# Performance work log

Measured on AMD Instinct MI355X. Metric: run time of the kernel, lower is better.

Reference implementation:

```python
import jax, jax.numpy as jnp
import numpy as np

DIM = 1024
HEADS = 16

def setup_inputs() -> dict:
    key = jax.random.key(0)
    ks = jax.random.split(key, 9)
    s = DIM ** -0.5  # init scale for weights
    x = jax.random.normal(ks[0], (2, 2048, DIM), dtype=jnp.float32)
    wq = jax.random.normal(ks[1], (DIM, DIM), dtype=jnp.float32) * s
    bq = jax.random.normal(ks[2], (DIM,), dtype=jnp.float32) * 0.01
    wk = jax.random.normal(ks[3], (DIM, DIM), dtype=jnp.float32) * s
    bk = jax.random.normal(ks[4], (DIM,), dtype=jnp.float32) * 0.01
    wv = jax.random.normal(ks[5], (DIM, DIM), dtype=jnp.float32) * s
    bv = jax.random.normal(ks[6], (DIM,), dtype=jnp.float32) * 0.01
    wo = jax.random.normal(ks[7], (DIM, DIM), dtype=jnp.float32) * s
    bo = jax.random.normal(ks[8], (DIM,), dtype=jnp.float32) * 0.01
    return {"x": x, "wq": wq, "bq": bq, "wk": wk, "bk": bk,
            "wv": wv, "bv": bv, "wo": wo, "bo": bo}

def reference(x, wq, bq, wk, bk, wv, bv, wo, bo):
    b, l, dim = x.shape
    h = HEADS
    d = dim // h
    scale = dim ** -0.5  # NOTE: full dim, as in the original module
    # torch Linear: x @ W.T + b
    def proj(w, bias):
        y = jnp.einsum('bld,ed->ble', x, w) + bias
        return y.reshape(b, l, h, d).transpose(0, 2, 1, 3)  # b h l d
    q = proj(wq, bq)
    k = proj(wk, bk)
    v = proj(wv, bv)
    attn = jnp.einsum('bhid,bhjd->bhij', q, k) * scale
    attn = jax.nn.softmax(attn, axis=-1)
    out = jnp.einsum('bhij,bhjd->bhid', attn, v)
    out = out.transpose(0, 2, 1, 3).reshape(b, l, dim)
    return jnp.einsum('ble,fe->blf', out, wo) + bo
```

## Files before the change

### kernel.cpp

```cpp
#include <hip/hip_runtime.h>
#include <hip/hip_bf16.h>
#include <stdint.h>


typedef __attribute__((ext_vector_type(8))) short short8;
typedef __attribute__((ext_vector_type(4))) float f32x4;
typedef __attribute__((ext_vector_type(16))) float f32x16;

#define MFMA(a, b, c) __builtin_amdgcn_mfma_f32_16x16x32_bf16((a), (b), (c), 0, 0, 0)
#define MFMA32(a, b, c) __builtin_amdgcn_mfma_f32_32x32x16_bf16((a), (b), (c), 0, 0, 0)

#if __has_builtin(__builtin_amdgcn_exp2f)
#define EXP2(x) __builtin_amdgcn_exp2f(x)
#else
#define EXP2(x) exp2f(x)
#endif

__device__ __forceinline__ ushort f2bf(float f) {
  uint32_t u = __builtin_bit_cast(uint32_t, f);
  u += 0x7fffu + ((u >> 16) & 1u);
  return (ushort)(u >> 16);
}

__device__ __forceinline__ uint32_t pkbf(float lo, float hi) {
  __hip_bfloat162 h = __float22bfloat162_rn(make_float2(lo, hi));
  uint32_t u;
  __builtin_memcpy(&u, &h, 4);
  return u;
}

__device__ __forceinline__ uint32_t cvtpk(float lo, float hi) {
  uint32_t u;
  asm("v_cvt_pk_bf16_f32 %0, %1, %2" : "=v"(u) : "v"(lo), "v"(hi));
  return u;
}

__device__ __forceinline__ void pl32swap(uint32_t& a, uint32_t& b) {
  asm("v_permlane32_swap_b32 %0, %1" : "+v"(a), "+v"(b));
}

__device__ __forceinline__ void gl_lds16(const void* g, void* l) {
  __builtin_amdgcn_global_load_lds(
      (const __attribute__((address_space(1))) unsigned int*)g,
      (__attribute__((address_space(3))) unsigned int*)l, 16, 0, 0);
}

__global__ __launch_bounds__(256) void convert_all(
    const float* __restrict__ x, const float* __restrict__ wq,
    const float* __restrict__ wk, const float* __restrict__ wv,
    const float* __restrict__ wo, ushort* __restrict__ dst) {
  size_t i4 = (size_t)blockIdx.x * 256 + threadIdx.x;
  size_t e = i4 * 4;
  const float* src; size_t off;
  if (e < 4194304u)      { src = x;  off = e; }
  else if (e < 5242880u) { src = wq; off = e - 4194304u; }
  else if (e < 6291456u) { src = wk; off = e - 5242880u; }
  else if (e < 7340032u) { src = wv; off = e - 6291456u; }
  else                   { src = wo; off = e - 7340032u; }
  float4 v = *(const float4*)(src + off);
  ushort4 o = { f2bf(v.x), f2bf(v.y), f2bf(v.z), f2bf(v.w) };
  *(ushort4*)(dst + e) = o;
}

__global__ __launch_bounds__(256) void gemm_qkv(
    const ushort* __restrict__ xb,
    const ushort* __restrict__ wqb, const ushort* __restrict__ wkb,
    const ushort* __restrict__ wvb,
    const float* __restrict__ bq_, const float* __restrict__ bk_,
    const float* __restrict__ bv_,
    ushort* __restrict__ qout, ushort* __restrict__ kout,
    ushort* __restrict__ vtout) {
  __shared__ __align__(16) ushort As[128 * 32];
  __shared__ __align__(16) ushort Bs[128 * 32];
  const int z = blockIdx.z;
  const int bn = blockIdx.x, bm = blockIdx.y;
  const int t = threadIdx.x;
  const int w = t >> 6, lane = t & 63;
  const int wr = w >> 1, wc = w & 1;
  const int l15 = lane & 15, l4 = lane >> 4;

  const ushort* wb = (z == 0) ? wqb : (z == 1 ? wkb : wvb);
  const float* bias = (z == 0) ? bq_ : (z == 1 ? bk_ : bv_);

  f32x4 acc[4][4] = {};

  for (int kt = 0; kt < 32; ++kt) {
    __syncthreads();
#pragma unroll
    for (int rr = 0; rr < 2; ++rr) {
      int c = t + rr * 256;
      int row = c >> 2, cin = c & 3;
      gl_lds16(xb + (bm * 128 + row) * 1024 + kt * 32 + cin * 8, (void*)&As[c * 8]);
      gl_lds16(wb + (bn * 128 + row) * 1024 + kt * 32 + cin * 8, (void*)&Bs[c * 8]);
    }
    __syncthreads();
    short8 af[4], bfr[4];
#pragma unroll
    for (int mf = 0; mf < 4; ++mf)
      af[mf] = *(const short8*)&As[(wr * 64 + mf * 16 + l15) * 32 + l4 * 8];
#pragma unroll
    for (int nf = 0; nf < 4; ++nf)
      bfr[nf] = *(const short8*)&Bs[(wc * 64 + nf * 16 + l15) * 32 + l4 * 8];
    __builtin_amdgcn_s_setprio(1);
#pragma unroll
    for (int mf = 0; mf < 4; ++mf)
#pragma unroll
      for (int nf = 0; nf < 4; ++nf)
        acc[mf][nf] = MFMA(af[mf], bfr[nf], acc[mf][nf]);
    __builtin_amdgcn_s_setprio(0);
  }

  const float qsc = 0.045084439f;
#pragma unroll
  for (int mf = 0; mf < 4; ++mf) {
#pragma unroll
    for (int nf = 0; nf < 4; ++nf) {
      int n = bn * 128 + wc * 64 + nf * 16 + l15;
      int m0 = bm * 128 + wr * 64 + mf * 16 + l4 * 4;
      float b = bias[n];
      float vals[4];
#pragma unroll
      for (int r = 0; r < 4; ++r) vals[r] = acc[mf][nf][r] + b;
      int bb = m0 >> 11, l0 = m0 & 2047;
      int h = n >> 6, d = n & 63;
      int bh = bb * 16 + h;
      if (z == 2) {
        *(uint2*)&vtout[(bh * 64 + d) * 2048 + l0] =
            make_uint2(pkbf(vals[0], vals[1]), pkbf(vals[2], vals[3]));
      } else if (z == 0) {
#pragma unroll
        for (int r = 0; r < 4; ++r)
          qout[(bh * 2048 + l0 + r) * 64 + d] = f2bf(vals[r] * qsc);
      } else {
#pragma unroll
        for (int r = 0; r < 4; ++r)
          kout[(bh * 2048 + l0 + r) * 64 + d] = f2bf(vals[r]);
      }
    }
  }
}

__global__ __launch_bounds__(256, 2) void attn(
    const ushort* __restrict__ qb, const ushort* __restrict__ kb,
    const ushort* __restrict__ vtb, ushort* __restrict__ aout) {
  __shared__ __align__(16) ushort Ks[2][64 * 64];
  __shared__ __align__(16) ushort Vs[2][64 * 64];
  const int bid = blockIdx.x;
  const int xcd = bid & 7, idx = bid >> 3;
  const int bh = xcd * 4 + (idx >> 4);
  const int it = idx & 15;
  const int t = threadIdx.x, w = t >> 6, lane = t & 63;
  const int l31 = lane & 31, hi = lane >> 5;
  const size_t kvbase = (size_t)bh * (2048 * 64);
  const int i0 = it * 128 + w * 32;

  const int c0 = t, c1 = t + 256;
  const int r0 = c0 >> 3, s0 = (c0 & 7) ^ (r0 & 7);
  const int r1 = c1 >> 3, s1 = (c1 & 7) ^ (r1 & 7);

#define STAGE(bufi, jts)                                                     \
  {                                                                          \
    const int j0s = (jts) * 64;                                              \
    gl_lds16(kb + kvbase + (size_t)(j0s + r0) * 64 + s0 * 8,                 \
             (void*)&Ks[bufi][c0 * 8]);                                      \
    gl_lds16(kb + kvbase + (size_t)(j0s + r1) * 64 + s1 * 8,                 \
             (void*)&Ks[bufi][c1 * 8]);                                      \
    gl_lds16(vtb + kvbase + (size_t)r0 * 2048 + j0s + s0 * 8,                \
             (void*)&Vs[bufi][c0 * 8]);                                      \
    gl_lds16(vtb + kvbase + (size_t)r1 * 2048 + j0s + s1 * 8,                \
             (void*)&Vs[bufi][c1 * 8]);                                      \
  }

  short8 qf[4];
#pragma unroll
  for (int ks = 0; ks < 4; ++ks)
    qf[ks] = *(const short8*)&qb[kvbase + (size_t)(i0 + l31) * 64 + ks * 16 + hi * 8];

  f32x16 ot0 = {}, ot1 = {};
  float ts0 = 0.f, ts1 = 0.f, ts2 = 0.f, ts3 = 0.f;

  STAGE(0, 0);
  __syncthreads();

  for (int jt = 0; jt < 32; ++jt) {
    const int cur = jt & 1;
    if (jt < 31) STAGE(cur ^ 1, jt + 1);

    const ushort* Kc = &Ks[cur][0];
    const ushort* Vc = &Vs[cur][0];

    const int swz = (l31 & 7);
    short8 ka0[4], ka1[4], va0[4], va1[4];
#pragma unroll
    for (int ks = 0; ks < 4; ++ks) {
      int ck = (ks * 2 + hi) ^ swz;
      ka0[ks] = *(const short8*)&Kc[l31 * 64 + ck * 8];
      ka1[ks] = *(const short8*)&Kc[(32 + l31) * 64 + ck * 8];
    }
#pragma unroll
    for (int b = 0; b < 4; ++b) {
      int cv = (b * 2 + hi) ^ swz;
      va0[b] = *(const short8*)&Vc[l31 * 64 + cv * 8];
      va1[b] = *(const short8*)&Vc[(32 + l31) * 64 + cv * 8];
    }

    f32x16 st0 = {}, st1 = {};
    __builtin_amdgcn_s_setprio(1);
#pragma unroll
    for (int ks = 0; ks < 4; ++ks) {
      st0 = MFMA32(ka0[ks], qf[ks], st0);
      st1 = MFMA32(ka1[ks], qf[ks], st1);
    }
    __builtin_amdgcn_s_setprio(0);

    f32x16 p0, p1;
#pragma unroll
    for (int r = 0; r < 16; r += 4) {
      p0[r] = EXP2(st0[r]);         ts0 += p0[r];
      p0[r + 1] = EXP2(st0[r + 1]); ts1 += p0[r + 1];
      p0[r + 2] = EXP2(st0[r + 2]); ts2 += p0[r + 2];
      p0[r + 3] = EXP2(st0[r + 3]); ts3 += p0[r + 3];
    }
#pragma unroll
    for (int r = 0; r < 16; r += 4) {
      p1[r] = EXP2(st1[r]);         ts0 += p1[r];
      p1[r + 1] = EXP2(st1[r + 1]); ts1 += p1[r + 1];
      p1[r + 2] = EXP2(st1[r + 2]); ts2 += p1[r + 2];
      p1[r + 3] = EXP2(st1[r + 3]); ts3 += p1[r + 3];
    }

    short8 pb[4];
#pragma unroll
    for (int b = 0; b < 4; ++b) {
      f32x16 pv = (b < 2) ? p0 : p1;
      const int R = 8 * (b & 1);
      uint32_t c01 = cvtpk(pv[R + 0], pv[R + 1]);
      uint32_t c23 = cvtpk(pv[R + 2], pv[R + 3]);
      uint32_t c45 = cvtpk(pv[R + 4], pv[R + 5]);
      uint32_t c67 = cvtpk(pv[R + 6], pv[R + 7]);
      pl32swap(c01, c45);
      pl32swap(c23, c67);
      union { uint32_t u[4]; short8 s; } pk;
      pk.u[0] = c01; pk.u[1] = c23; pk.u[2] = c45; pk.u[3] = c67;
      pb[b] = pk.s;
    }

    __builtin_amdgcn_s_setprio(1);
#pragma unroll
    for (int b = 0; b < 4; ++b) {
      ot0 = MFMA32(va0[b], pb[b], ot0);
      ot1 = MFMA32(va1[b], pb[b], ot1);
    }
    __builtin_amdgcn_s_setprio(0);

    __syncthreads();
  }

  float lsum = (ts0 + ts1) + (ts2 + ts3);
  {
    uint32_t a = __builtin_bit_cast(uint32_t, lsum);
    uint32_t b = a;
    pl32swap(a, b);
    lsum = __builtin_bit_cast(float, a) + __builtin_bit_cast(float, b);
  }
  const int bb = bh >> 4, h = bh & 15;
  float inv = 1.0f / lsum;
  ushort* orow = aout + (size_t)(bb * 2048 + i0 + l31) * 1024 + h * 64;
#pragma unroll
  for (int mf = 0; mf < 2; ++mf) {
    f32x16 o = mf ? ot1 : ot0;
#pragma unroll
    for (int g = 0; g < 4; ++g) {
      int d0 = mf * 32 + g * 8 + hi * 4;
      *(uint2*)(orow + d0) = make_uint2(
          cvtpk(o[g * 4 + 0] * inv, o[g * 4 + 1] * inv),
          cvtpk(o[g * 4 + 2] * inv, o[g * 4 + 3] * inv));
    }
  }
#undef STAGE
}

__global__ __launch_bounds__(256) void gemm_out(
    const ushort* __restrict__ ab, const ushort* __restrict__ wob,
    const float* __restrict__ bo_, float* __restrict__ out) {
  __shared__ __align__(16) ushort As[128 * 32];
  __shared__ __align__(16) ushort Bs[128 * 32];
  const int bn = blockIdx.x, bm = blockIdx.y;
  const int t = threadIdx.x;
  const int w = t >> 6, lane = t & 63;
  const int wr = w >> 1, wc = w & 1;
  const int l15 = lane & 15, l4 = lane >> 4;

  f32x4 acc[4][4] = {};

  for (int kt = 0; kt < 32; ++kt) {
    __syncthreads();
#pragma unroll
    for (int rr = 0; rr < 2; ++rr) {
      int c = t + rr * 256;
      int row = c >> 2, cin = c & 3;
      gl_lds16(ab + (bm * 128 + row) * 1024 + kt * 32 + cin * 8, (void*)&As[c * 8]);
      gl_lds16(wob + (bn * 128 + row) * 1024 + kt * 32 + cin * 8, (void*)&Bs[c * 8]);
    }
    __syncthreads();
    short8 af[4], bfr[4];
#pragma unroll
    for (int mf = 0; mf < 4; ++mf)
      af[mf] = *(const short8*)&As[(wr * 64 + mf * 16 + l15) * 32 + l4 * 8];
#pragma unroll
    for (int nf = 0; nf < 4; ++nf)
      bfr[nf] = *(const short8*)&Bs[(wc * 64 + nf * 16 + l15) * 32 + l4 * 8];
    __builtin_amdgcn_s_setprio(1);
#pragma unroll
    for (int mf = 0; mf < 4; ++mf)
#pragma unroll
      for (int nf = 0; nf < 4; ++nf)
        acc[mf][nf] = MFMA(af[mf], bfr[nf], acc[mf][nf]);
    __builtin_amdgcn_s_setprio(0);
  }

#pragma unroll
  for (int mf = 0; mf < 4; ++mf)
#pragma unroll
    for (int nf = 0; nf < 4; ++nf) {
      int n = bn * 128 + wc * 64 + nf * 16 + l15;
      int m0 = bm * 128 + wr * 64 + mf * 16 + l4 * 4;
      float b = bo_[n];
#pragma unroll
      for (int r = 0; r < 4; ++r)
        out[(size_t)(m0 + r) * 1024 + n] = acc[mf][nf][r] + b;
    }
}

extern "C" void kernel_launch(void* const* d_in, const int* in_sizes, int n_in,
                              void* d_out, int out_size, void* d_ws, size_t ws_size,
                              hipStream_t stream) {
  const float* x  = (const float*)d_in[0];
  const float* wq = (const float*)d_in[1];
  const float* bq = (const float*)d_in[2];
  const float* wk = (const float*)d_in[3];
  const float* bk = (const float*)d_in[4];
  const float* wv = (const float*)d_in[5];
  const float* bv = (const float*)d_in[6];
  const float* wo = (const float*)d_in[7];
  const float* bo = (const float*)d_in[8];

  ushort* ws  = (ushort*)d_ws;
  ushort* xb  = ws;
  ushort* wqb = ws + 4194304;
  ushort* wkb = ws + 5242880;
  ushort* wvb = ws + 6291456;
  ushort* wob = ws + 7340032;
  ushort* qbp = ws + 8388608;
  ushort* kbp = ws + 12582912;
  ushort* vtb = ws + 16777216;
  ushort* ab  = ws + 20971520;

  convert_all<<<8192, 256, 0, stream>>>(x, wq, wk, wv, wo, ws);
  gemm_qkv<<<dim3(8, 32, 3), 256, 0, stream>>>(xb, wqb, wkb, wvb, bq, bk, bv,
                                               qbp, kbp, vtb);
  attn<<<512, 256, 0, stream>>>(qbp, kbp, vtb, ab);
  gemm_out<<<dim3(8, 32), 256, 0, stream>>>(ab, wob, bo, (float*)d_out);
}
```

Before: 113.7 us.

## Split attention KV range across warp pairs and double the grid

Each attention block now covers 64 query rows instead of 128. Its four warps form two row groups, and each group's two warps take different halves of the KV sequence (split-K). The launch doubles to 1024 blocks and the launch bound asks for 4 blocks per CU, to raise occupancy and parallelism. Partial outputs and softmax sums are reduced through LDS at the end, which adds a sync and a shared-memory reduction. K/V staging is rewritten to load both halves into one buffer, and each warp now does half the MFMAs per tile. K/V traffic per query row grows because each block reloads the full KV for fewer rows.

```diff
diff --git a/kernel.cpp b/kernel.cpp
--- a/kernel.cpp
+++ b/kernel.cpp
@@ -140,35 +140,36 @@
   }
 }
 
-__global__ __launch_bounds__(256, 2) void attn(
+__global__ __launch_bounds__(256, 4) void attn(
     const ushort* __restrict__ qb, const ushort* __restrict__ kb,
     const ushort* __restrict__ vtb, ushort* __restrict__ aout) {
   __shared__ __align__(16) ushort Ks[2][64 * 64];
   __shared__ __align__(16) ushort Vs[2][64 * 64];
   const int bid = blockIdx.x;
   const int xcd = bid & 7, idx = bid >> 3;
-  const int bh = xcd * 4 + (idx >> 4);
-  const int it = idx & 15;
+  const int bh = xcd * 4 + (idx >> 5);
+  const int it = idx & 31;
   const int t = threadIdx.x, w = t >> 6, lane = t & 63;
   const int l31 = lane & 31, hi = lane >> 5;
+  const int rg = w & 1;
+  const int half = w >> 1;
   const size_t kvbase = (size_t)bh * (2048 * 64);
-  const int i0 = it * 128 + w * 32;
-
-  const int c0 = t, c1 = t + 256;
-  const int r0 = c0 >> 3, s0 = (c0 & 7) ^ (r0 & 7);
-  const int r1 = c1 >> 3, s1 = (c1 & 7) ^ (r1 & 7);
+  const int i0 = it * 64 + rg * 32;
 
 #define STAGE(bufi, jts)                                                     \
   {                                                                          \
-    const int j0s = (jts) * 64;                                              \
-    gl_lds16(kb + kvbase + (size_t)(j0s + r0) * 64 + s0 * 8,                 \
-             (void*)&Ks[bufi][c0 * 8]);                                      \
-    gl_lds16(kb + kvbase + (size_t)(j0s + r1) * 64 + s1 * 8,                 \
-             (void*)&Ks[bufi][c1 * 8]);                                      \
-    gl_lds16(vtb + kvbase + (size_t)r0 * 2048 + j0s + s0 * 8,                \
-             (void*)&Vs[bufi][c0 * 8]);                                      \
-    gl_lds16(vtb + kvbase + (size_t)r1 * 2048 + j0s + s1 * 8,                \
-             (void*)&Vs[bufi][c1 * 8]);                                      \
+    const int jb0 = (jts) * 32, jb1 = 1024 + (jts) * 32;                     \
+    _Pragma("unroll")                                                        \
+    for (int rr = 0; rr < 2; ++rr) {                                         \
+      int c = t + rr * 256;                                                  \
+      int r = c >> 3, o = (c & 7) ^ (r & 7);                                 \
+      int jr = (r < 32) ? (jb0 + r) : (jb1 + r - 32);                        \
+      gl_lds16(kb + kvbase + (size_t)jr * 64 + o * 8,                        \
+               (void*)&Ks[bufi][c * 8]);                                     \
+      int jc = (o < 4) ? (jb0 + o * 8) : (jb1 + (o - 4) * 8);                \
+      gl_lds16(vtb + kvbase + (size_t)r * 2048 + jc,                         \
+               (void*)&Vs[bufi][c * 8]);                                     \
+    }                                                                        \
   }
 
   short8 qf[4];
@@ -178,6 +179,8 @@
 
   f32x16 ot0 = {}, ot1 = {};
   float ts0 = 0.f, ts1 = 0.f, ts2 = 0.f, ts3 = 0.f;
+  const int swz = l31 & 7;
+  const int rowk = half * 32 + l31;
 
   STAGE(0, 0);
   __syncthreads();
@@ -189,67 +192,54 @@
     const ushort* Kc = &Ks[cur][0];
     const ushort* Vc = &Vs[cur][0];
 
-    const int swz = (l31 & 7);
-    short8 ka0[4], ka1[4], va0[4], va1[4];
+    short8 ka[4], va0[2], va1[2];
 #pragma unroll
     for (int ks = 0; ks < 4; ++ks) {
       int ck = (ks * 2 + hi) ^ swz;
-      ka0[ks] = *(const short8*)&Kc[l31 * 64 + ck * 8];
-      ka1[ks] = *(const short8*)&Kc[(32 + l31) * 64 + ck * 8];
-    }
-#pragma unroll
-    for (int b = 0; b < 4; ++b) {
-      int cv = (b * 2 + hi) ^ swz;
-      va0[b] = *(const short8*)&Vc[l31 * 64 + cv * 8];
-      va1[b] = *(const short8*)&Vc[(32 + l31) * 64 + cv * 8];
-    }
-
-    f32x16 st0 = {}, st1 = {};
+      ka[ks] = *(const short8*)&Kc[rowk * 64 + ck * 8];
+    }
+#pragma unroll
+    for (int s = 0; s < 2; ++s) {
+      int cv = (half * 4 + s * 2 + hi) ^ swz;
+      va0[s] = *(const short8*)&Vc[l31 * 64 + cv * 8];
+      va1[s] = *(const short8*)&Vc[(32 + l31) * 64 + cv * 8];
+    }
+
+    f32x16 st = {};
     __builtin_amdgcn_s_setprio(1);
 #pragma unroll
-    for (int ks = 0; ks < 4; ++ks) {
-      st0 = MFMA32(ka0[ks], qf[ks], st0);
-      st1 = MFMA32(ka1[ks], qf[ks], st1);
-    }
+    for (int ks = 0; ks < 4; ++ks) st = MFMA32(ka[ks], qf[ks], st);
     __builtin_amdgcn_s_setprio(0);
 
-    f32x16 p0, p1;
+    f32x16 p;
 #pragma unroll
     for (int r = 0; r < 16; r += 4) {
-      p0[r] = EXP2(st0[r]);         ts0 += p0[r];
-      p0[r + 1] = EXP2(st0[r + 1]); ts1 += p0[r + 1];
-      p0[r + 2] = EXP2(st0[r + 2]); ts2 += p0[r + 2];
-      p0[r + 3] = EXP2(st0[r + 3]); ts3 += p0[r + 3];
-    }
-#pragma unroll
-    for (int r = 0; r < 16; r += 4) {
-      p1[r] = EXP2(st1[r]);         ts0 += p1[r];
-      p1[r + 1] = EXP2(st1[r + 1]); ts1 += p1[r + 1];
-      p1[r + 2] = EXP2(st1[r + 2]); ts2 += p1[r + 2];
-      p1[r + 3] = EXP2(st1[r + 3]); ts3 += p1[r + 3];
-    }
-
-    short8 pb[4];
-#pragma unroll
-    for (int b = 0; b < 4; ++b) {
-      f32x16 pv = (b < 2) ? p0 : p1;
-      const int R = 8 * (b & 1);
-      uint32_t c01 = cvtpk(pv[R + 0], pv[R + 1]);
-      uint32_t c23 = cvtpk(pv[R + 2], pv[R + 3]);
-      uint32_t c45 = cvtpk(pv[R + 4], pv[R + 5]);
-      uint32_t c67 = cvtpk(pv[R + 6], pv[R + 7]);
+      p[r] = EXP2(st[r]);         ts0 += p[r];
+      p[r + 1] = EXP2(st[r + 1]); ts1 += p[r + 1];
+      p[r + 2] = EXP2(st[r + 2]); ts2 += p[r + 2];
+      p[r + 3] = EXP2(st[r + 3]); ts3 += p[r + 3];
+    }
+
+    short8 pb[2];
+#pragma unroll
+    for (int s = 0; s < 2; ++s) {
+      const int R = 8 * s;
+      uint32_t c01 = cvtpk(p[R + 0], p[R + 1]);
+      uint32_t c23 = cvtpk(p[R + 2], p[R + 3]);
+      uint32_t c45 = cvtpk(p[R + 4], p[R + 5]);
+      uint32_t c67 = cvtpk(p[R + 6], p[R + 7]);
       pl32swap(c01, c45);
       pl32swap(c23, c67);
-      union { uint32_t u[4]; short8 s; } pk;
+      union { uint32_t u[4]; short8 s8; } pk;
       pk.u[0] = c01; pk.u[1] = c23; pk.u[2] = c45; pk.u[3] = c67;
-      pb[b] = pk.s;
+      pb[s] = pk.s8;
     }
 
     __builtin_amdgcn_s_setprio(1);
 #pragma unroll
-    for (int b = 0; b < 4; ++b) {
-      ot0 = MFMA32(va0[b], pb[b], ot0);
-      ot1 = MFMA32(va1[b], pb[b], ot1);
+    for (int s = 0; s < 2; ++s) {
+      ot0 = MFMA32(va0[s], pb[s], ot0);
+      ot1 = MFMA32(va1[s], pb[s], ot1);
     }
     __builtin_amdgcn_s_setprio(0);
 
@@ -257,24 +247,49 @@
   }
 
   float lsum = (ts0 + ts1) + (ts2 + ts3);
-  {
+  float* sh = (float*)&Ks[0][0];
+  float* base = sh + rg * 2560;
+  if (half == 1) {
+#pragma unroll
+    for (int g = 0; g < 4; ++g) {
+      f32x4 q0 = { ot0[g * 4], ot0[g * 4 + 1], ot0[g * 4 + 2], ot0[g * 4 + 3] };
+      f32x4 q1 = { ot1[g * 4], ot1[g * 4 + 1], ot1[g * 4 + 2], ot1[g * 4 + 3] };
+      *(f32x4*)&base[lane * 40 + g * 4] = q0;
+      *(f32x4*)&base[lane * 40 + 16 + g * 4] = q1;
+    }
+    base[lane * 40 + 32] = lsum;
+  }
+  __syncthreads();
+  if (half == 0) {
+#pragma unroll
+    for (int g = 0; g < 4; ++g) {
+      f32x4 q0 = *(const f32x4*)&base[lane * 40 + g * 4];
+      f32x4 q1 = *(const f32x4*)&base[lane * 40 + 16 + g * 4];
+#pragma unroll
+      for (int e = 0; e < 4; ++e) {
+        ot0[g * 4 + e] += q0[e];
+        ot1[g * 4 + e] += q1[e];
+      }
+    }
+    lsum += base[lane * 40 + 32];
     uint32_t a = __builtin_bit_cast(uint32_t, lsum);
     uint32_t b = a;
     pl32swap(a, b);
     lsum = __builtin_bit_cast(float, a) + __builtin_bit_cast(float, b);
-  }
-  const int bb = bh >> 4, h = bh & 15;
-  float inv = 1.0f / lsum;
-  ushort* orow = aout + (size_t)(bb * 2048 + i0 + l31) * 1024 + h * 64;
-#pragma unroll
-  for (int mf = 0; mf < 2; ++mf) {
-    f32x16 o = mf ? ot1 : ot0;
-#pragma unroll
-    for (int g = 0; g < 4; ++g) {
-      int d0 = mf * 32 + g * 8 + hi * 4;
-      *(uint2*)(orow + d0) = make_uint2(
-          cvtpk(o[g * 4 + 0] * inv, o[g * 4 + 1] * inv),
-          cvtpk(o[g * 4 + 2] * inv, o[g * 4 + 3] * inv));
+
+    const int bb = bh >> 4, h = bh & 15;
+    float inv = 1.0f / lsum;
+    ushort* orow = aout + (size_t)(bb * 2048 + i0 + l31) * 1024 + h * 64;
+#pragma unroll
+    for (int mf = 0; mf < 2; ++mf) {
+      f32x16 o = mf ? ot1 : ot0;
+#pragma unroll
+      for (int g = 0; g < 4; ++g) {
+        int d0 = mf * 32 + g * 8 + hi * 4;
+        *(uint2*)(orow + d0) = make_uint2(
+            cvtpk(o[g * 4 + 0] * inv, o[g * 4 + 1] * inv),
+            cvtpk(o[g * 4 + 2] * inv, o[g * 4 + 3] * inv));
+      }
     }
   }
 #undef STAGE
@@ -359,6 +374,6 @@
   convert_all<<<8192, 256, 0, stream>>>(x, wq, wk, wv, wo, ws);
   gemm_qkv<<<dim3(8, 32, 3), 256, 0, stream>>>(xb, wqb, wkb, wvb, bq, bk, bv,
                                                qbp, kbp, vtb);
-  attn<<<512, 256, 0, stream>>>(qbp, kbp, vtb, ab);
+  attn<<<1024, 256, 0, stream>>>(qbp, kbp, vtb, ab);
   gemm_out<<<dim3(8, 32), 256, 0, stream>>>(ab, wob, bo, (float*)d_out);
 }
```

After: 119.6 us. 5.2% more time.
